# Performance work log

Measured on AMD Instinct MI355X. Metric: run time of the kernel, lower is better.

Reference implementation:

```python
import jax, jax.numpy as jnp
import numpy as np

B, T, C, H = 8, 2048, 1024, 128

def setup_inputs() -> dict:
    key = jax.random.key(0)
    kx, kq, kk, kv = jax.random.split(key, 4)
    x = jax.random.normal(kx, (B, T, C), dtype=jnp.float32)
    Wq = jax.random.normal(kq, (C, H), dtype=jnp.float32) * 0.02
    Wk = jax.random.normal(kk, (C, H), dtype=jnp.float32) * 0.02
    Wv = jax.random.normal(kv, (C, H), dtype=jnp.float32) * 0.02
    return {"x": x, "Wq": Wq, "Wk": Wk, "Wv": Wv}

def reference(x, Wq, Wk, Wv):
    # q,k,v: [B,T,H] via bias-free dense projections
    q = jnp.einsum('btc,ch->bth', x, Wq)
    k = jnp.einsum('btc,ch->bth', x, Wk)
    v = jnp.einsum('btc,ch->bth', x, Wv)
    scale = k.shape[-1] ** (-0.5)
    # scores: [B,T,T]
    wei = jnp.einsum('bth,bsh->bts', q, k) * scale
    Tlen = x.shape[1]
    causal = jnp.tril(jnp.ones((Tlen, Tlen), dtype=bool))  # True = keep
    wei = jnp.where(causal[None, :, :], wei, -jnp.inf)
    wei = jax.nn.softmax(wei, axis=-1)
    return jnp.einsum('bts,bsh->bth', wei, v)
```

## Files before the change

### kernel.cpp

```cpp
#include <hip/hip_runtime.h>

#define B_ 8
#define T_ 2048
#define C_ 1024
#define H_ 128
#define BT_ (B_*T_)

typedef unsigned short u16;
typedef unsigned int u32;
typedef __attribute__((ext_vector_type(4))) float f32x4;
typedef __attribute__((ext_vector_type(8))) __bf16 bf16x8;

__device__ __forceinline__ u16 f2bf(float f) {
  u32 u = __float_as_uint(f);
  u += 0x7fffu + ((u >> 16) & 1u);
  return (u16)(u >> 16);
}

#define GLL16(g, l) __builtin_amdgcn_global_load_lds( \
    (const __attribute__((address_space(1))) void*)(g), \
    (__attribute__((address_space(3))) void*)(l), 16, 0, 0)

__device__ __forceinline__ bf16x8 load_frag(const u16* base, int stride, int row0, int k0, int lane) {
  const u16* p = base + (size_t)(row0 + (lane & 15)) * stride + k0 + ((lane >> 4) << 3);
  return *reinterpret_cast<const bf16x8*>(p);
}

__device__ __forceinline__ bf16x8 cvt8n(f32x4 lo, f32x4 hi) {
  bf16x8 r;
#pragma unroll
  for (int i = 0; i < 4; i++) { r[i] = (__bf16)lo[i]; r[4 + i] = (__bf16)hi[i]; }
  return r;
}

__global__ void wt_kernel(const float* __restrict__ Wq, const float* __restrict__ Wk,
                          const float* __restrict__ Wv, u16* __restrict__ wt) {
  int mat = blockIdx.y;
  const float* W = (mat == 0) ? Wq : (mat == 1) ? Wk : Wv;
  int i = blockIdx.x * 256 + threadIdx.x;
  int h = i >> 10;
  int c = i & 1023;
  wt[mat * (C_ * H_) + i] = f2bf(W[c * H_ + h]);
}

__global__ __launch_bounds__(512, 4) void qkv_gemm(const float* __restrict__ x, const u16* __restrict__ wt,
                                                   u16* __restrict__ q, u16* __restrict__ k2,
                                                   u16* __restrict__ vt) {
  __shared__ __align__(16) float As[2][64 * 64];
  __shared__ __align__(16) u16 Bs[2][192 * 64];
  int t = threadIdx.x;
  int lane = t & 63, w = t >> 6;
  int wm = w >> 2, wn = w & 3;
  int quad = lane >> 4, col = lane & 15;
  int m0 = blockIdx.x * 64;
  int nb = blockIdx.y * 192;

  int arow = t >> 4;
  int acg = (t & 15) ^ (arow & 15);
  const float* ax0 = x + (size_t)(m0 + arow) * C_ + acg * 4;
  const float* ax1 = ax0 + (size_t)32 * C_;
  int brow = t >> 3;
  int bcg = (t & 7) ^ (brow & 7);
  const u16* bw0 = wt + (size_t)(nb + brow) * C_ + bcg * 8;
  const u16* bw1 = bw0 + (size_t)64 * C_;
  const u16* bw2 = bw0 + (size_t)128 * C_;

#define STAGE(st, buf) do { \
    int ko_ = (st) * 64; \
    GLL16(ax0 + ko_, &As[buf][t * 4]); \
    GLL16(ax1 + ko_, &As[buf][2048 + t * 4]); \
    GLL16(bw0 + ko_, &Bs[buf][t * 8]); \
    GLL16(bw1 + ko_, &Bs[buf][4096 + t * 8]); \
    GLL16(bw2 + ko_, &Bs[buf][8192 + t * 8]); \
  } while (0)

  STAGE(0, 0);

  f32x4 acc[2][3] = {};
#pragma unroll 2
  for (int kk = 0; kk < 16; kk++) {
    int cur = kk & 1;
    __syncthreads();
    if (kk + 1 < 16) STAGE(kk + 1, cur ^ 1);
    const float* Ab = &As[cur][0];
    const u16* Bb = &Bs[cur][0];
#pragma unroll
    for (int ks = 0; ks < 2; ks++) {
      bf16x8 af[2], bfr[3];
#pragma unroll
      for (int mt = 0; mt < 2; mt++) {
        int rr = wm * 32 + mt * 16 + col;
        int s0 = (ks * 8 + quad * 2) ^ (rr & 15);
        int s1 = s0 ^ 1;
        f32x4 lo = *reinterpret_cast<const f32x4*>(Ab + rr * 64 + s0 * 4);
        f32x4 hi = *reinterpret_cast<const f32x4*>(Ab + rr * 64 + s1 * 4);
        af[mt] = cvt8n(lo, hi);
      }
#pragma unroll
      for (int nt = 0; nt < 3; nt++) {
        int rr = wn * 48 + nt * 16 + col;
        int sl = (ks * 4 + quad) ^ (rr & 7);
        bfr[nt] = *reinterpret_cast<const bf16x8*>(Bb + rr * 64 + sl * 8);
      }
#pragma unroll
      for (int mt = 0; mt < 2; mt++)
#pragma unroll
        for (int nt = 0; nt < 3; nt++)
          acc[mt][nt] = __builtin_amdgcn_mfma_f32_16x16x32_bf16(af[mt], bfr[nt], acc[mt][nt], 0, 0, 0);
    }
  }
#undef STAGE

#pragma unroll
  for (int mt = 0; mt < 2; mt++) {
    int row0 = m0 + wm * 32 + mt * 16 + quad * 4;
#pragma unroll
    for (int nt = 0; nt < 3; nt++) {
      int n = nb + wn * 48 + nt * 16 + col;
      int mat = n >> 7, h = n & 127;
      if (mat == 0) {
#pragma unroll
        for (int r = 0; r < 4; r++) q[(size_t)(row0 + r) * H_ + h] = f2bf(acc[mt][nt][r]);
      } else if (mat == 1) {
#pragma unroll
        for (int r = 0; r < 4; r++) k2[(size_t)(row0 + r) * H_ + h] = f2bf(acc[mt][nt][r]);
      } else {
        int bb = row0 >> 11, tt = row0 & 2047;
        ushort4 pk;
        pk.x = f2bf(acc[mt][nt][0]); pk.y = f2bf(acc[mt][nt][1]);
        pk.z = f2bf(acc[mt][nt][2]); pk.w = f2bf(acc[mt][nt][3]);
        *reinterpret_cast<ushort4*>(&vt[((size_t)bb * H_ + h) * T_ + tt]) = pk;
      }
    }
  }
}

__global__ __launch_bounds__(256, 4) void attn_part(const u16* __restrict__ q, const u16* __restrict__ k,
                                                    const u16* __restrict__ vt,
                                                    float* __restrict__ Op, float* __restrict__ lsum) {
  __shared__ __align__(16) u16 Ks[2][32 * 132];
  __shared__ __align__(16) u16 Vs[2][128 * 36];
  __shared__ __align__(16) u16 P[4][16 * 40];
  int t = threadIdx.x;
  int lane = t & 63, w = t >> 6;
  int quad = lane >> 4, col = lane & 15;
  int bx = blockIdx.x;
  int qt = 31 - (bx >> 5);
  int s = (bx >> 3) & 3;
  int b = bx & 7;
  const float scale = 0.08838834764831845f;

  int nk = 2 * (qt + 1);
  int it0 = (s * nk) >> 2;
  int it1 = ((s + 1) * nk) >> 2;

  int krow0 = t >> 4, ke = (t & 15) * 8;
  int krow1 = krow0 + 16;
  int vrow0 = t >> 2, ve = (t & 3) * 8;
  int vrow1 = vrow0 + 64;

  int qrow0 = b * T_ + qt * 64 + w * 16;
  bf16x8 qf[4];
#pragma unroll
  for (int ks = 0; ks < 4; ks++) qf[ks] = load_frag(q, H_, qrow0, ks * 32, lane);

  f32x4 o[8] = {};
  float l[4] = {0.f, 0.f, 0.f, 0.f};
  int myqrow = qt * 64 + w * 16 + quad * 4;

  if (it0 < it1) {
    const u16* kb = k + (size_t)(b * T_ + it0 * 32) * H_;
    *reinterpret_cast<uint4*>(&Ks[0][krow0 * 132 + ke]) = *reinterpret_cast<const uint4*>(kb + (size_t)krow0 * 128 + ke);
    *reinterpret_cast<uint4*>(&Ks[0][krow1 * 132 + ke]) = *reinterpret_cast<const uint4*>(kb + (size_t)krow1 * 128 + ke);
    const u16* vb = vt + (size_t)b * H_ * T_ + it0 * 32;
    *reinterpret_cast<uint4*>(&Vs[0][vrow0 * 36 + ve]) = *reinterpret_cast<const uint4*>(vb + (size_t)vrow0 * T_ + ve);
    *reinterpret_cast<uint4*>(&Vs[0][vrow1 * 36 + ve]) = *reinterpret_cast<const uint4*>(vb + (size_t)vrow1 * T_ + ve);
  }

  for (int kt = it0; kt < it1; kt++) {
    int cur = (kt - it0) & 1;
    __syncthreads();
    bool more = (kt + 1 < it1);
    uint4 kc0, kc1, vc0, vc1;
    if (more) {
      const u16* kb = k + (size_t)(b * T_ + (kt + 1) * 32) * H_;
      kc0 = *reinterpret_cast<const uint4*>(kb + (size_t)krow0 * 128 + ke);
      kc1 = *reinterpret_cast<const uint4*>(kb + (size_t)krow1 * 128 + ke);
      const u16* vb = vt + (size_t)b * H_ * T_ + (kt + 1) * 32;
      vc0 = *reinterpret_cast<const uint4*>(vb + (size_t)vrow0 * T_ + ve);
      vc1 = *reinterpret_cast<const uint4*>(vb + (size_t)vrow1 * T_ + ve);
    }

    f32x4 s0 = {}, s1 = {};
#pragma unroll
    for (int ks = 0; ks < 4; ks++) {
      bf16x8 kb0 = *reinterpret_cast<const bf16x8*>(&Ks[cur][col * 132 + ks * 32 + quad * 8]);
      bf16x8 kb1 = *reinterpret_cast<const bf16x8*>(&Ks[cur][(col + 16) * 132 + ks * 32 + quad * 8]);
      s0 = __builtin_amdgcn_mfma_f32_16x16x32_bf16(qf[ks], kb0, s0, 0, 0, 0);
      s1 = __builtin_amdgcn_mfma_f32_16x16x32_bf16(qf[ks], kb1, s1, 0, 0, 0);
    }

    float pv[8];
    int kcol0 = kt * 32 + col;
#pragma unroll
    for (int r = 0; r < 4; r++) {
      int qr = myqrow + r;
      float a0 = fminf(s0[r] * scale, 30.f);
      float a1 = fminf(s1[r] * scale, 30.f);
      a0 = (kcol0      > qr) ? -1e30f : a0;
      a1 = (kcol0 + 16 > qr) ? -1e30f : a1;
      float p0 = __expf(a0);
      float p1 = __expf(a1);
      pv[r] = p0; pv[4 + r] = p1;
      l[r] += p0 + p1;
    }

    u16* Pb = &P[w][0];
#pragma unroll
    for (int r = 0; r < 4; r++) {
      Pb[(quad * 4 + r) * 40 + col] = f2bf(pv[r]);
      Pb[(quad * 4 + r) * 40 + col + 16] = f2bf(pv[4 + r]);
    }
    asm volatile("" ::: "memory");
    __builtin_amdgcn_s_waitcnt(0xc07f);
    asm volatile("" ::: "memory");
    bf16x8 pf = *reinterpret_cast<const bf16x8*>(&Pb[col * 40 + (quad << 3)]);

#pragma unroll
    for (int ht = 0; ht < 8; ht++) {
      bf16x8 vf = *reinterpret_cast<const bf16x8*>(&Vs[cur][(ht * 16 + col) * 36 + quad * 8]);
      o[ht] = __builtin_amdgcn_mfma_f32_16x16x32_bf16(pf, vf, o[ht], 0, 0, 0);
    }

    if (more) {
      int nxt = cur ^ 1;
      *reinterpret_cast<uint4*>(&Ks[nxt][krow0 * 132 + ke]) = kc0;
      *reinterpret_cast<uint4*>(&Ks[nxt][krow1 * 132 + ke]) = kc1;
      *reinterpret_cast<uint4*>(&Vs[nxt][vrow0 * 36 + ve]) = vc0;
      *reinterpret_cast<uint4*>(&Vs[nxt][vrow1 * 36 + ve]) = vc1;
    }
  }

#pragma unroll
  for (int r = 0; r < 4; r++) {
    float v = l[r];
    v += __shfl_xor(v, 1);
    v += __shfl_xor(v, 2);
    v += __shfl_xor(v, 4);
    v += __shfl_xor(v, 8);
    l[r] = v;
  }

  int tile = (s * 8 + b) * 32 + qt;
  float* Orow = Op + (size_t)tile * (64 * 128);
  float* lrow = lsum + (size_t)tile * 64;
  int rowin0 = w * 16 + quad * 4;
  if (col == 0) {
#pragma unroll
    for (int r = 0; r < 4; r++) lrow[rowin0 + r] = l[r];
  }
#pragma unroll
  for (int ht = 0; ht < 8; ht++) {
#pragma unroll
    for (int r = 0; r < 4; r++)
      Orow[(size_t)(rowin0 + r) * 128 + ht * 16 + col] = o[ht][r];
  }
}

__global__ __launch_bounds__(256) void attn_comb(const float* __restrict__ Op, const float* __restrict__ lsum,
                                                 float* __restrict__ out) {
  int bx = blockIdx.x;
  int b = bx >> 5, qt = bx & 31;
  int t = threadIdx.x;
  int h = t & 127, half = t >> 7;
  int tile0 = b * 32 + qt;
#pragma unroll 4
  for (int rr = 0; rr < 32; rr++) {
    int row = half * 32 + rr;
    float ls = 0.f, v = 0.f;
#pragma unroll
    for (int p = 0; p < 4; p++) {
      int tp = tile0 + p * 256;
      ls += lsum[tp * 64 + row];
      v  += Op[(size_t)tp * 8192 + row * 128 + h];
    }
    out[((size_t)(b * T_ + qt * 64 + row)) * H_ + h] = v / ls;
  }
}

extern "C" void kernel_launch(void* const* d_in, const int* in_sizes, int n_in,
                              void* d_out, int out_size, void* d_ws, size_t ws_size,
                              hipStream_t stream) {
  (void)in_sizes; (void)n_in; (void)out_size; (void)ws_size;
  const float* x  = (const float*)d_in[0];
  const float* Wq = (const float*)d_in[1];
  const float* Wk = (const float*)d_in[2];
  const float* Wv = (const float*)d_in[3];
  u16* ws = (u16*)d_ws;
  u16* q  = ws;
  u16* k  = ws + (size_t)BT_ * H_;
  u16* vt = ws + 2 * (size_t)BT_ * H_;
  u16* wt = ws + 3 * (size_t)BT_ * H_;
  float* Op = (float*)(ws + 3 * (size_t)BT_ * H_ + 3 * C_ * H_);
  float* lsum = Op + (size_t)1024 * 64 * 128;
  float* out = (float*)d_out;

  wt_kernel<<<dim3(512, 3), 256, 0, stream>>>(Wq, Wk, Wv, wt);
  qkv_gemm<<<dim3(BT_ / 64, 2), 512, 0, stream>>>(x, wt, q, k, vt);
  attn_part<<<dim3(1024), 256, 0, stream>>>(q, k, vt, Op, lsum);
  attn_comb<<<dim3(256), 256, 0, stream>>>(Op, lsum, out);
}
```

Measured before the change: 152.2 us.

## Enlarge attention query tile to 128 rows with 8 waves per block

The partial-attention kernel now processes 128 query rows per block using 512 threads (8 wavefronts), so each K/V tile staged in LDS is reused by twice as many queries. Each thread now loads one K and one V vector per tile instead of two, and the split of the key range into four parts is simplified to equal chunks of qt+1 tiles. The combine kernel and workspace layout are adjusted for 128-row tiles. This halves the block count, which may reduce occupancy and load balance across CUs, and the causal split is coarser.

```diff
diff --git a/kernel.cpp b/kernel.cpp
--- a/kernel.cpp
+++ b/kernel.cpp
@@ -135,60 +135,53 @@
   }
 }
 
-__global__ __launch_bounds__(256, 4) void attn_part(const u16* __restrict__ q, const u16* __restrict__ k,
+__global__ __launch_bounds__(512, 4) void attn_part(const u16* __restrict__ q, const u16* __restrict__ k,
                                                     const u16* __restrict__ vt,
                                                     float* __restrict__ Op, float* __restrict__ lsum) {
   __shared__ __align__(16) u16 Ks[2][32 * 132];
   __shared__ __align__(16) u16 Vs[2][128 * 36];
-  __shared__ __align__(16) u16 P[4][16 * 40];
+  __shared__ __align__(16) u16 P[8][16 * 40];
   int t = threadIdx.x;
   int lane = t & 63, w = t >> 6;
   int quad = lane >> 4, col = lane & 15;
   int bx = blockIdx.x;
-  int qt = 31 - (bx >> 5);
+  int qt = 15 - (bx >> 5);
   int s = (bx >> 3) & 3;
   int b = bx & 7;
   const float scale = 0.08838834764831845f;
 
-  int nk = 2 * (qt + 1);
-  int it0 = (s * nk) >> 2;
-  int it1 = ((s + 1) * nk) >> 2;
-
-  int krow0 = t >> 4, ke = (t & 15) * 8;
-  int krow1 = krow0 + 16;
-  int vrow0 = t >> 2, ve = (t & 3) * 8;
-  int vrow1 = vrow0 + 64;
-
-  int qrow0 = b * T_ + qt * 64 + w * 16;
+  int it0 = s * (qt + 1);
+  int it1 = it0 + (qt + 1);
+
+  int krow = t >> 4, ke = (t & 15) * 8;
+  int vrow = t >> 2, ve = (t & 3) * 8;
+
+  int qrow0 = b * T_ + qt * 128 + w * 16;
   bf16x8 qf[4];
 #pragma unroll
   for (int ks = 0; ks < 4; ks++) qf[ks] = load_frag(q, H_, qrow0, ks * 32, lane);
 
   f32x4 o[8] = {};
   float l[4] = {0.f, 0.f, 0.f, 0.f};
-  int myqrow = qt * 64 + w * 16 + quad * 4;
-
-  if (it0 < it1) {
+  int myqrow = qt * 128 + w * 16 + quad * 4;
+
+  {
     const u16* kb = k + (size_t)(b * T_ + it0 * 32) * H_;
-    *reinterpret_cast<uint4*>(&Ks[0][krow0 * 132 + ke]) = *reinterpret_cast<const uint4*>(kb + (size_t)krow0 * 128 + ke);
-    *reinterpret_cast<uint4*>(&Ks[0][krow1 * 132 + ke]) = *reinterpret_cast<const uint4*>(kb + (size_t)krow1 * 128 + ke);
+    *reinterpret_cast<uint4*>(&Ks[0][krow * 132 + ke]) = *reinterpret_cast<const uint4*>(kb + (size_t)krow * 128 + ke);
     const u16* vb = vt + (size_t)b * H_ * T_ + it0 * 32;
-    *reinterpret_cast<uint4*>(&Vs[0][vrow0 * 36 + ve]) = *reinterpret_cast<const uint4*>(vb + (size_t)vrow0 * T_ + ve);
-    *reinterpret_cast<uint4*>(&Vs[0][vrow1 * 36 + ve]) = *reinterpret_cast<const uint4*>(vb + (size_t)vrow1 * T_ + ve);
+    *reinterpret_cast<uint4*>(&Vs[0][vrow * 36 + ve]) = *reinterpret_cast<const uint4*>(vb + (size_t)vrow * T_ + ve);
   }
 
   for (int kt = it0; kt < it1; kt++) {
     int cur = (kt - it0) & 1;
     __syncthreads();
     bool more = (kt + 1 < it1);
-    uint4 kc0, kc1, vc0, vc1;
+    uint4 kc, vc;
     if (more) {
       const u16* kb = k + (size_t)(b * T_ + (kt + 1) * 32) * H_;
-      kc0 = *reinterpret_cast<const uint4*>(kb + (size_t)krow0 * 128 + ke);
-      kc1 = *reinterpret_cast<const uint4*>(kb + (size_t)krow1 * 128 + ke);
+      kc = *reinterpret_cast<const uint4*>(kb + (size_t)krow * 128 + ke);
       const u16* vb = vt + (size_t)b * H_ * T_ + (kt + 1) * 32;
-      vc0 = *reinterpret_cast<const uint4*>(vb + (size_t)vrow0 * T_ + ve);
-      vc1 = *reinterpret_cast<const uint4*>(vb + (size_t)vrow1 * T_ + ve);
+      vc = *reinterpret_cast<const uint4*>(vb + (size_t)vrow * T_ + ve);
     }
 
     f32x4 s0 = {}, s1 = {};
@@ -234,10 +227,8 @@
 
     if (more) {
       int nxt = cur ^ 1;
-      *reinterpret_cast<uint4*>(&Ks[nxt][krow0 * 132 + ke]) = kc0;
-      *reinterpret_cast<uint4*>(&Ks[nxt][krow1 * 132 + ke]) = kc1;
-      *reinterpret_cast<uint4*>(&Vs[nxt][vrow0 * 36 + ve]) = vc0;
-      *reinterpret_cast<uint4*>(&Vs[nxt][vrow1 * 36 + ve]) = vc1;
+      *reinterpret_cast<uint4*>(&Ks[nxt][krow * 132 + ke]) = kc;
+      *reinterpret_cast<uint4*>(&Vs[nxt][vrow * 36 + ve]) = vc;
     }
   }
 
@@ -251,9 +242,9 @@
     l[r] = v;
   }
 
-  int tile = (s * 8 + b) * 32 + qt;
-  float* Orow = Op + (size_t)tile * (64 * 128);
-  float* lrow = lsum + (size_t)tile * 64;
+  int tile = (s * 8 + b) * 16 + qt;
+  float* Orow = Op + (size_t)tile * (128 * 128);
+  float* lrow = lsum + (size_t)tile * 128;
   int rowin0 = w * 16 + quad * 4;
   if (col == 0) {
 #pragma unroll
@@ -270,21 +261,21 @@
 __global__ __launch_bounds__(256) void attn_comb(const float* __restrict__ Op, const float* __restrict__ lsum,
                                                  float* __restrict__ out) {
   int bx = blockIdx.x;
-  int b = bx >> 5, qt = bx & 31;
+  int b = bx >> 4, qt = bx & 15;
   int t = threadIdx.x;
   int h = t & 127, half = t >> 7;
-  int tile0 = b * 32 + qt;
+  int tile0 = b * 16 + qt;
 #pragma unroll 4
-  for (int rr = 0; rr < 32; rr++) {
-    int row = half * 32 + rr;
+  for (int rr = 0; rr < 64; rr++) {
+    int row = half * 64 + rr;
     float ls = 0.f, v = 0.f;
 #pragma unroll
     for (int p = 0; p < 4; p++) {
-      int tp = tile0 + p * 256;
-      ls += lsum[tp * 64 + row];
-      v  += Op[(size_t)tp * 8192 + row * 128 + h];
-    }
-    out[((size_t)(b * T_ + qt * 64 + row)) * H_ + h] = v / ls;
+      int tp = tile0 + p * 128;
+      ls += lsum[tp * 128 + row];
+      v  += Op[(size_t)tp * 16384 + row * 128 + h];
+    }
+    out[((size_t)(b * T_ + qt * 128 + row)) * H_ + h] = v / ls;
   }
 }
 
@@ -302,11 +293,11 @@
   u16* vt = ws + 2 * (size_t)BT_ * H_;
   u16* wt = ws + 3 * (size_t)BT_ * H_;
   float* Op = (float*)(ws + 3 * (size_t)BT_ * H_ + 3 * C_ * H_);
-  float* lsum = Op + (size_t)1024 * 64 * 128;
+  float* lsum = Op + (size_t)512 * 128 * 128;
   float* out = (float*)d_out;
 
   wt_kernel<<<dim3(512, 3), 256, 0, stream>>>(Wq, Wk, Wv, wt);
   qkv_gemm<<<dim3(BT_ / 64, 2), 512, 0, stream>>>(x, wt, q, k, vt);
-  attn_part<<<dim3(1024), 256, 0, stream>>>(q, k, vt, Op, lsum);
-  attn_comb<<<dim3(256), 256, 0, stream>>>(Op, lsum, out);
-}
+  attn_part<<<dim3(512), 512, 0, stream>>>(q, k, vt, Op, lsum);
+  attn_comb<<<dim3(128), 256, 0, stream>>>(Op, lsum, out);
+}
```

After: 157.9 us. +3.8%, slower.
